# Optimization experiments

Measured on AMD Instinct MI355X. Metric: run time of the kernel, lower is better.

Reference implementation:

```python
import jax, jax.numpy as jnp
import numpy as np

NEG = 1e12  # matches the torch '-inf' surrogate value


def _sinusoidal_pos(seq_len, dim):
    # bert4keras-style: pe[..., 0::2] = sin, pe[..., 1::2] = cos
    pos = jnp.arange(seq_len, dtype=jnp.float32)
    i = jnp.arange(dim // 2, dtype=jnp.float32)
    freq = jnp.power(10000.0, -2.0 * i / dim)
    ang = pos[:, None] * freq[None, :]                      # [S, dim/2]
    pe = jnp.stack([jnp.sin(ang), jnp.cos(ang)], axis=-1)   # [S, dim/2, 2]
    return pe.reshape(seq_len, dim)                          # [S, dim]


def _rope(e, cos_pos, sin_pos):
    # additional_part = stack([-e[...,1::2], e[...,::2]], -1).reshape(e.shape)
    rot = jnp.stack([-e[..., 1::2], e[..., 0::2]], axis=-1).reshape(e.shape)
    return e * cos_pos + rot * sin_pos


def setup_inputs() -> dict:
    key = jax.random.key(0)
    k = jax.random.split(key, 5)
    B, S, H, inner, L = 8, 512, 768, 64, 16
    x = jax.random.normal(k[0], (B, S, H), dtype=jnp.float32)
    W1 = jax.random.normal(k[1], (H, 2 * inner), dtype=jnp.float32) * 0.02
    b1 = jnp.zeros((2 * inner,), dtype=jnp.float32)
    W2 = jax.random.normal(k[2], (H, 2 * L), dtype=jnp.float32) * 0.02
    b2 = jnp.zeros((2 * L,), dtype=jnp.float32)
    attention_mask = jnp.ones((B, S), dtype=jnp.int32)
    return {"x": x, "W1": W1, "b1": b1, "W2": W2, "b2": b2,
            "attention_mask": attention_mask}


def reference(x, W1, b1, W2, b2, attention_mask):
    B, S, H = x.shape
    inner = W1.shape[1] // 2

    t = x @ W1 + b1                                 # [B,S,2*inner]
    start_token = t[..., 0::2]                      # [B,S,inner]
    end_token = t[..., 1::2]                        # [B,S,inner]

    pe = _sinusoidal_pos(S, inner)[None]            # [1,S,inner]
    cos_pos = jnp.repeat(pe[..., 1::2], 2, axis=-1)
    sin_pos = jnp.repeat(pe[..., 0::2], 2, axis=-1)
    start_token = _rope(start_token, cos_pos, sin_pos)
    end_token = _rope(end_token, cos_pos, sin_pos)

    span_score = jnp.einsum('bmd,bnd->bmn', start_token, end_token) / (inner ** 0.5)

    typing = jnp.swapaxes(x @ W2 + b2, 1, 2) / 2.0  # [B,2L,S]

    # entity_score: [B, L, S(start), S(end)]
    entity_score = (span_score[:, None]
                    + typing[:, 0::2, None, :]
                    + typing[:, 1::2, :, None])

    m = attention_mask.astype(entity_score.dtype)
    m_row = m[:, None, :, None]                     # mask over start axis
    m_col = m[:, None, None, :]                     # mask over end axis
    entity_score = entity_score * m_row + (-NEG) * (1.0 - m_row)
    entity_score = entity_score * m_col + (-NEG) * (1.0 - m_col)

    tril = jnp.tril(jnp.ones((S, S), entity_score.dtype), k=-1)
    entity_score = entity_score - tril * NEG
    return entity_score
```

## Files before the change

kernel.cpp:

```cpp
#include <hip/hip_runtime.h>

#define NEGF 1.0e12f

constexpr int Hdim = 768;
constexpr int NC   = 160;
constexpr int ROWS = 4096;
constexpr int SEQ  = 512;
constexpr int KSPLIT = 4;

typedef __attribute__((ext_vector_type(8))) short  short8;
typedef __attribute__((ext_vector_type(4))) float  floatx4;

__device__ inline unsigned short f2bf(float f) {
    union { float f; unsigned u; } v; v.f = f;
    return (unsigned short)((v.u + 0x8000u) >> 16);
}

__global__ __launch_bounds__(256) void wprep_k(
    const float* __restrict__ W1, const float* __restrict__ W2,
    unsigned short* __restrict__ Wt)
{
    __shared__ __align__(16) unsigned short tile[160][72];
    const int tid = threadIdx.x;
    const int k0  = blockIdx.x * 64;

    for (int t = tid; t < 64 * 32; t += 256) {
        int k  = t >> 5;
        int c4 = (t & 31) * 4;
        float4 v = *(const float4*)(W1 + (size_t)(k0 + k) * 128 + c4);
        tile[c4 + 0][k] = f2bf(v.x); tile[c4 + 1][k] = f2bf(v.y);
        tile[c4 + 2][k] = f2bf(v.z); tile[c4 + 3][k] = f2bf(v.w);
    }
    for (int t = tid; t < 64 * 8; t += 256) {
        int k  = t >> 3;
        int c4 = (t & 7) * 4;
        float4 v = *(const float4*)(W2 + (size_t)(k0 + k) * 32 + c4);
        tile[128 + c4 + 0][k] = f2bf(v.x); tile[128 + c4 + 1][k] = f2bf(v.y);
        tile[128 + c4 + 2][k] = f2bf(v.z); tile[128 + c4 + 3][k] = f2bf(v.w);
    }
    __syncthreads();
    for (int t = tid; t < 160 * 8; t += 256) {
        int c  = t >> 3;
        int kq = (t & 7) * 8;
        short8 v = *(const short8*)(&tile[c][kq]);
        *(short8*)(Wt + (size_t)c * 768 + k0 + kq) = v;
    }
}

__global__ __launch_bounds__(256) void gemm_mfma_k(
    const float* __restrict__ x, const unsigned short* __restrict__ Wt,
    float* __restrict__ partial)
{
    __shared__ __align__(16) unsigned short xs[64 * 40];
    __shared__ __align__(16) unsigned short ws[NC * 40];

    const int tid  = threadIdx.x;
    const int wave = tid >> 6;
    const int lane = tid & 63;
    const int quad = lane >> 4;
    const int nl   = lane & 15;
    const int r0   = blockIdx.x * 64;
    const int k0   = blockIdx.y * 192;

    floatx4 acc[10];
#pragma unroll
    for (int t = 0; t < 10; t++) acc[t] = (floatx4)(0.0f);

    for (int kt = 0; kt < 192; kt += 32) {
        const int kb = k0 + kt;
        {
            const int row = tid >> 2;
            const int kq  = (tid & 3) * 8;
            const float* xp = x + (size_t)(r0 + row) * Hdim + kb + kq;
            float4 v0 = *(const float4*)xp;
            float4 v1 = *(const float4*)(xp + 4);
            short8 sv;
            sv[0] = (short)f2bf(v0.x); sv[1] = (short)f2bf(v0.y);
            sv[2] = (short)f2bf(v0.z); sv[3] = (short)f2bf(v0.w);
            sv[4] = (short)f2bf(v1.x); sv[5] = (short)f2bf(v1.y);
            sv[6] = (short)f2bf(v1.z); sv[7] = (short)f2bf(v1.w);
            *(short8*)(xs + row * 40 + kq) = sv;
        }
#pragma unroll
        for (int g = 0; g < 3; g++) {
            int task = g * 256 + tid;
            if (task < 640) {
                int c  = task >> 2;
                int kq = (task & 3) * 8;
                *(short8*)(ws + c * 40 + kq) =
                    *(const short8*)(Wt + (size_t)c * 768 + kb + kq);
            }
        }
        __syncthreads();

        short8 af = *(const short8*)(xs + (wave * 16 + nl) * 40 + quad * 8);
#pragma unroll
        for (int t = 0; t < 10; t++) {
            short8 bf = *(const short8*)(ws + (t * 16 + nl) * 40 + quad * 8);
            acc[t] = __builtin_amdgcn_mfma_f32_16x16x32_bf16(af, bf, acc[t], 0, 0, 0);
        }
        __syncthreads();
    }

    float* pout = partial + (size_t)blockIdx.y * ROWS * NC;
#pragma unroll
    for (int t = 0; t < 10; t++) {
#pragma unroll
        for (int r = 0; r < 4; r++) {
            pout[(size_t)(r0 + wave * 16 + quad * 4 + r) * NC + t * 16 + nl] = acc[t][r];
        }
    }
}

__global__ __launch_bounds__(256) void combine_rope_k(
    const float* __restrict__ partial, const float* __restrict__ b1,
    const float* __restrict__ b2, unsigned short* __restrict__ startbf,
    unsigned short* __restrict__ endbf, float* __restrict__ tyn,
    float* __restrict__ tym)
{
    const int tid = threadIdx.x;
    const int row = blockIdx.x * 4 + (tid >> 6);
    const int u   = tid & 63;
    const int b   = row >> 9;
    const int s   = row & 511;
    const float* p0 = partial + (size_t)row * NC;
    const size_t cstride = (size_t)ROWS * NC;

    if (u < 32) {
        const int i = u;
        float4 a0 = *(const float4*)(p0 + 4 * i);
        float4 a1 = *(const float4*)(p0 + cstride + 4 * i);
        float4 a2 = *(const float4*)(p0 + 2 * cstride + 4 * i);
        float4 a3 = *(const float4*)(p0 + 3 * cstride + 4 * i);
        float t0 = a0.x + a1.x + a2.x + a3.x + b1[4 * i + 0];
        float t1 = a0.y + a1.y + a2.y + a3.y + b1[4 * i + 1];
        float t2 = a0.z + a1.z + a2.z + a3.z + b1[4 * i + 2];
        float t3 = a0.w + a1.w + a2.w + a3.w + b1[4 * i + 3];
        float freq = __powf(10000.0f, -(float)i * (1.0f / 32.0f));
        float ang  = (float)s * freq;
        float sn, cs;
        __sincosf(ang, &sn, &cs);
        float so0 = (t0 * cs - t2 * sn) * 0.125f;
        float so1 = (t2 * cs + t0 * sn) * 0.125f;
        float eo0 = t1 * cs - t3 * sn;
        float eo1 = t3 * cs + t1 * sn;
        ushort2 sp; sp.x = f2bf(so0); sp.y = f2bf(so1);
        ushort2 ep; ep.x = f2bf(eo0); ep.y = f2bf(eo1);
        *(ushort2*)(startbf + (size_t)row * 64 + 2 * i) = sp;
        *(ushort2*)(endbf   + (size_t)row * 64 + 2 * i) = ep;
    } else {
        const int j = u - 32;
        float t = p0[128 + j] + p0[cstride + 128 + j] + p0[2 * cstride + 128 + j]
                + p0[3 * cstride + 128 + j] + b2[j];
        float v = t * 0.5f;
        const int l = j >> 1;
        if ((j & 1) == 0) tyn[((size_t)b * 16 + l) * SEQ + s] = v;
        else              tym[((size_t)b * 16 + l) * SEQ + s] = v;
    }
}

__global__ __launch_bounds__(256) void entity_k(
    const unsigned short* __restrict__ startbf, const unsigned short* __restrict__ endbf,
    const float* __restrict__ tyn, const float* __restrict__ tym,
    const int* __restrict__ amask, float* __restrict__ out)
{
    __shared__ __align__(16) unsigned short sA[64 * 72];
    __shared__ __align__(16) unsigned short sB[64 * 72];
    __shared__ float tyn_s[16 * 64];
    __shared__ float tym_s[16 * 64];
    __shared__ float mrow_s[64];
    __shared__ float mcol_s[64];

    const int tid = threadIdx.x;
    const int b   = blockIdx.z;
    const int m0  = blockIdx.y * 64;
    const int n0  = blockIdx.x * 64;

    for (int t = tid; t < 512; t += 256) {
        int row = t >> 3;
        int kq  = (t & 7) * 8;
        *(short8*)(sA + row * 72 + kq) =
            *(const short8*)(startbf + (size_t)(b * SEQ + m0 + row) * 64 + kq);
        *(short8*)(sB + row * 72 + kq) =
            *(const short8*)(endbf + (size_t)(b * SEQ + n0 + row) * 64 + kq);
    }
    for (int t = tid; t < 16 * 64; t += 256) {
        int l = t >> 6, i = t & 63;
        tym_s[t] = tym[((size_t)b * 16 + l) * SEQ + m0 + i];
        tyn_s[t] = tyn[((size_t)b * 16 + l) * SEQ + n0 + i];
    }
    if (tid < 64)       mrow_s[tid] = (float)amask[b * SEQ + m0 + tid];
    else if (tid < 128) mcol_s[tid - 64] = (float)amask[b * SEQ + n0 + (tid - 64)];
    __syncthreads();

    const int wave = tid >> 6;
    const int lane = tid & 63;
    const int quad = lane >> 4;
    const int nl   = lane & 15;

    short8 a0 = *(const short8*)(sA + (wave * 16 + nl) * 72 + quad * 8);
    short8 a1 = *(const short8*)(sA + (wave * 16 + nl) * 72 + 32 + quad * 8);

    floatx4 acc[4];
#pragma unroll
    for (int t = 0; t < 4; t++) acc[t] = (floatx4)(0.0f);
#pragma unroll
    for (int t = 0; t < 4; t++) {
        short8 bf0 = *(const short8*)(sB + (t * 16 + nl) * 72 + quad * 8);
        short8 bf1 = *(const short8*)(sB + (t * 16 + nl) * 72 + 32 + quad * 8);
        acc[t] = __builtin_amdgcn_mfma_f32_16x16x32_bf16(a0, bf0, acc[t], 0, 0, 0);
        acc[t] = __builtin_amdgcn_mfma_f32_16x16x32_bf16(a1, bf1, acc[t], 0, 0, 0);
    }

    float mr[4], radd[4];
#pragma unroll
    for (int r = 0; r < 4; r++) {
        mr[r]   = mrow_s[wave * 16 + quad * 4 + r];
        radd[r] = -NEGF * (1.0f - mr[r]);
    }
    float mc[4], cadd[4];
#pragma unroll
    for (int t = 0; t < 4; t++) {
        mc[t]   = mcol_s[t * 16 + nl];
        cadd[t] = -NEGF * (1.0f - mc[t]);
    }
    const bool lower = (m0 > n0);
    const bool diag  = (m0 == n0);
    const int  lm    = wave * 16 + quad * 4;

    for (int l = 0; l < 16; l++) {
        float tmv[4];
#pragma unroll
        for (int r = 0; r < 4; r++) tmv[r] = tym_s[l * 64 + lm + r];
        float* ob = out + ((size_t)(b * 16 + l) * SEQ + m0 + lm) * SEQ + n0;
#pragma unroll
        for (int t = 0; t < 4; t++) {
            float tnv = tyn_s[l * 64 + t * 16 + nl];
#pragma unroll
            for (int r = 0; r < 4; r++) {
                float v = acc[t][r] + tnv + tmv[r];
                v = v * mr[r] + radd[r];
                v = v * mc[t] + cadd[t];
                if (lower) v -= NEGF;
                else if (diag && (lm + r > t * 16 + nl)) v -= NEGF;
                ob[(size_t)r * SEQ + t * 16 + nl] = v;
            }
        }
    }
}

extern "C" void kernel_launch(void* const* d_in, const int* in_sizes, int n_in,
                              void* d_out, int out_size, void* d_ws, size_t ws_size,
                              hipStream_t stream) {
    const float* x     = (const float*)d_in[0];
    const float* W1    = (const float*)d_in[1];
    const float* b1    = (const float*)d_in[2];
    const float* W2    = (const float*)d_in[3];
    const float* b2    = (const float*)d_in[4];
    const int*   amask = (const int*)d_in[5];
    float* out = (float*)d_out;

    char* base = (char*)d_ws;
    unsigned short* Wt      = (unsigned short*)base;
    float*          partial = (float*)(base + 262144);
    unsigned short* startbf = (unsigned short*)(base + 262144 + 10485760);
    unsigned short* endbf   = (unsigned short*)(base + 262144 + 10485760 + 524288);
    float*          tyn     = (float*)(base + 262144 + 10485760 + 2 * 524288);
    float*          tym     = (float*)(base + 262144 + 10485760 + 2 * 524288 + 262144);

    hipLaunchKernelGGL(wprep_k, dim3(12), dim3(256), 0, stream, W1, W2, Wt);
    hipLaunchKernelGGL(gemm_mfma_k, dim3(64, KSPLIT), dim3(256), 0, stream,
                       x, Wt, partial);
    hipLaunchKernelGGL(combine_rope_k, dim3(ROWS / 4), dim3(256), 0, stream,
                       partial, b1, b2, startbf, endbf, tyn, tym);
    hipLaunchKernelGGL(entity_k, dim3(8, 8, 8), dim3(256), 0, stream,
                       startbf, endbf, tyn, tym, amask, out);
}
```

Before: 177.4 us.

## Fuse split-K projection GEMM with RoPE combine and drop LDS staging in entity kernel

The projection GEMM now splits K across the 8 waves of one block and reduces the partials in shared memory, then applies bias, RoPE and typing scaling in the same kernel. This removes the 10 MB partial buffer round-trip through global memory and one kernel launch. The entity kernel now loads its MFMA operands, typing values and mask directly from global memory into registers instead of staging them in LDS behind a barrier. The trade-off is only 256 GEMM blocks, each doing a small amount of work, and uncoalesced, repeated global reads in the entity kernel that rely on cache hits.

```diff
diff --git a/kernel.cpp b/kernel.cpp
--- a/kernel.cpp
+++ b/kernel.cpp
@@ -6,7 +6,6 @@
 constexpr int NC   = 160;
 constexpr int ROWS = 4096;
 constexpr int SEQ  = 512;
-constexpr int KSPLIT = 4;
 
 typedef __attribute__((ext_vector_type(8))) short  short8;
 typedef __attribute__((ext_vector_type(4))) float  floatx4;
@@ -47,115 +46,96 @@
     }
 }
 
-__global__ __launch_bounds__(256) void gemm_mfma_k(
+__global__ __launch_bounds__(512) void gemm_rope_k(
     const float* __restrict__ x, const unsigned short* __restrict__ Wt,
-    float* __restrict__ partial)
+    const float* __restrict__ b1, const float* __restrict__ b2,
+    unsigned short* __restrict__ startbf, unsigned short* __restrict__ endbf,
+    float* __restrict__ tyn, float* __restrict__ tym)
 {
-    __shared__ __align__(16) unsigned short xs[64 * 40];
-    __shared__ __align__(16) unsigned short ws[NC * 40];
+    __shared__ __align__(16) float ts[8 * 16 * 160];
 
     const int tid  = threadIdx.x;
     const int wave = tid >> 6;
     const int lane = tid & 63;
     const int quad = lane >> 4;
     const int nl   = lane & 15;
-    const int r0   = blockIdx.x * 64;
-    const int k0   = blockIdx.y * 192;
+    const int r0   = blockIdx.x * 16;
+    const int kbase = wave * 96;
 
     floatx4 acc[10];
 #pragma unroll
     for (int t = 0; t < 10; t++) acc[t] = (floatx4)(0.0f);
 
-    for (int kt = 0; kt < 192; kt += 32) {
-        const int kb = k0 + kt;
-        {
-            const int row = tid >> 2;
-            const int kq  = (tid & 3) * 8;
-            const float* xp = x + (size_t)(r0 + row) * Hdim + kb + kq;
-            float4 v0 = *(const float4*)xp;
-            float4 v1 = *(const float4*)(xp + 4);
-            short8 sv;
-            sv[0] = (short)f2bf(v0.x); sv[1] = (short)f2bf(v0.y);
-            sv[2] = (short)f2bf(v0.z); sv[3] = (short)f2bf(v0.w);
-            sv[4] = (short)f2bf(v1.x); sv[5] = (short)f2bf(v1.y);
-            sv[6] = (short)f2bf(v1.z); sv[7] = (short)f2bf(v1.w);
-            *(short8*)(xs + row * 40 + kq) = sv;
+#pragma unroll
+    for (int it = 0; it < 3; it++) {
+        const int kw = kbase + it * 32;
+        const float* xp = x + (size_t)(r0 + nl) * Hdim + kw + quad * 8;
+        float4 xa = *(const float4*)xp;
+        float4 xb = *(const float4*)(xp + 4);
+        short8 wr[10];
+#pragma unroll
+        for (int t = 0; t < 10; t++)
+            wr[t] = *(const short8*)(Wt + (size_t)(t * 16 + nl) * Hdim + kw + quad * 8);
+
+        short8 af;
+        af[0] = (short)f2bf(xa.x); af[1] = (short)f2bf(xa.y);
+        af[2] = (short)f2bf(xa.z); af[3] = (short)f2bf(xa.w);
+        af[4] = (short)f2bf(xb.x); af[5] = (short)f2bf(xb.y);
+        af[6] = (short)f2bf(xb.z); af[7] = (short)f2bf(xb.w);
+#pragma unroll
+        for (int t = 0; t < 10; t++)
+            acc[t] = __builtin_amdgcn_mfma_f32_16x16x32_bf16(af, wr[t], acc[t], 0, 0, 0);
+    }
+
+#pragma unroll
+    for (int t = 0; t < 10; t++) {
+#pragma unroll
+        for (int r = 0; r < 4; r++) {
+            ts[(wave * 16 + quad * 4 + r) * 160 + t * 16 + nl] = acc[t][r];
         }
-#pragma unroll
-        for (int g = 0; g < 3; g++) {
-            int task = g * 256 + tid;
-            if (task < 640) {
-                int c  = task >> 2;
-                int kq = (task & 3) * 8;
-                *(short8*)(ws + c * 40 + kq) =
-                    *(const short8*)(Wt + (size_t)c * 768 + kb + kq);
+    }
+    __syncthreads();
+
+#pragma unroll
+    for (int p = 0; p < 2; p++) {
+        const int unit = tid + p * 512;
+        const int lrow = unit >> 6;
+        const int u    = unit & 63;
+        const int grow = r0 + lrow;
+        const int b    = grow >> 9;
+        const int s    = grow & 511;
+        if (u < 32) {
+            const int i = u;
+            float t0 = 0.0f, t1 = 0.0f, t2 = 0.0f, t3 = 0.0f;
+#pragma unroll
+            for (int w = 0; w < 8; w++) {
+                float4 v = *(const float4*)(ts + (w * 16 + lrow) * 160 + 4 * i);
+                t0 += v.x; t1 += v.y; t2 += v.z; t3 += v.w;
             }
+            float4 bv = *(const float4*)(b1 + 4 * i);
+            t0 += bv.x; t1 += bv.y; t2 += bv.z; t3 += bv.w;
+            float freq = __powf(10000.0f, -(float)i * (1.0f / 32.0f));
+            float ang  = (float)s * freq;
+            float sn, cs;
+            __sincosf(ang, &sn, &cs);
+            float so0 = (t0 * cs - t2 * sn) * 0.125f;
+            float so1 = (t2 * cs + t0 * sn) * 0.125f;
+            float eo0 = t1 * cs - t3 * sn;
+            float eo1 = t3 * cs + t1 * sn;
+            ushort2 sp; sp.x = f2bf(so0); sp.y = f2bf(so1);
+            ushort2 ep; ep.x = f2bf(eo0); ep.y = f2bf(eo1);
+            *(ushort2*)(startbf + (size_t)grow * 64 + 2 * i) = sp;
+            *(ushort2*)(endbf   + (size_t)grow * 64 + 2 * i) = ep;
+        } else {
+            const int j = u - 32;
+            float t = 0.0f;
+#pragma unroll
+            for (int w = 0; w < 8; w++) t += ts[(w * 16 + lrow) * 160 + 128 + j];
+            float v = (t + b2[j]) * 0.5f;
+            const int l = j >> 1;
+            if ((j & 1) == 0) tyn[((size_t)b * 16 + l) * SEQ + s] = v;
+            else              tym[((size_t)b * 16 + l) * SEQ + s] = v;
         }
-        __syncthreads();
-
-        short8 af = *(const short8*)(xs + (wave * 16 + nl) * 40 + quad * 8);
-#pragma unroll
-        for (int t = 0; t < 10; t++) {
-            short8 bf = *(const short8*)(ws + (t * 16 + nl) * 40 + quad * 8);
-            acc[t] = __builtin_amdgcn_mfma_f32_16x16x32_bf16(af, bf, acc[t], 0, 0, 0);
-        }
-        __syncthreads();
-    }
-
-    float* pout = partial + (size_t)blockIdx.y * ROWS * NC;
-#pragma unroll
-    for (int t = 0; t < 10; t++) {
-#pragma unroll
-        for (int r = 0; r < 4; r++) {
-            pout[(size_t)(r0 + wave * 16 + quad * 4 + r) * NC + t * 16 + nl] = acc[t][r];
-        }
-    }
-}
-
-__global__ __launch_bounds__(256) void combine_rope_k(
-    const float* __restrict__ partial, const float* __restrict__ b1,
-    const float* __restrict__ b2, unsigned short* __restrict__ startbf,
-    unsigned short* __restrict__ endbf, float* __restrict__ tyn,
-    float* __restrict__ tym)
-{
-    const int tid = threadIdx.x;
-    const int row = blockIdx.x * 4 + (tid >> 6);
-    const int u   = tid & 63;
-    const int b   = row >> 9;
-    const int s   = row & 511;
-    const float* p0 = partial + (size_t)row * NC;
-    const size_t cstride = (size_t)ROWS * NC;
-
-    if (u < 32) {
-        const int i = u;
-        float4 a0 = *(const float4*)(p0 + 4 * i);
-        float4 a1 = *(const float4*)(p0 + cstride + 4 * i);
-        float4 a2 = *(const float4*)(p0 + 2 * cstride + 4 * i);
-        float4 a3 = *(const float4*)(p0 + 3 * cstride + 4 * i);
-        float t0 = a0.x + a1.x + a2.x + a3.x + b1[4 * i + 0];
-        float t1 = a0.y + a1.y + a2.y + a3.y + b1[4 * i + 1];
-        float t2 = a0.z + a1.z + a2.z + a3.z + b1[4 * i + 2];
-        float t3 = a0.w + a1.w + a2.w + a3.w + b1[4 * i + 3];
-        float freq = __powf(10000.0f, -(float)i * (1.0f / 32.0f));
-        float ang  = (float)s * freq;
-        float sn, cs;
-        __sincosf(ang, &sn, &cs);
-        float so0 = (t0 * cs - t2 * sn) * 0.125f;
-        float so1 = (t2 * cs + t0 * sn) * 0.125f;
-        float eo0 = t1 * cs - t3 * sn;
-        float eo1 = t3 * cs + t1 * sn;
-        ushort2 sp; sp.x = f2bf(so0); sp.y = f2bf(so1);
-        ushort2 ep; ep.x = f2bf(eo0); ep.y = f2bf(eo1);
-        *(ushort2*)(startbf + (size_t)row * 64 + 2 * i) = sp;
-        *(ushort2*)(endbf   + (size_t)row * 64 + 2 * i) = ep;
-    } else {
-        const int j = u - 32;
-        float t = p0[128 + j] + p0[cstride + 128 + j] + p0[2 * cstride + 128 + j]
-                + p0[3 * cstride + 128 + j] + b2[j];
-        float v = t * 0.5f;
-        const int l = j >> 1;
-        if ((j & 1) == 0) tyn[((size_t)b * 16 + l) * SEQ + s] = v;
-        else              tym[((size_t)b * 16 + l) * SEQ + s] = v;
     }
 }
 
@@ -164,82 +144,64 @@
     const float* __restrict__ tyn, const float* __restrict__ tym,
     const int* __restrict__ amask, float* __restrict__ out)
 {
-    __shared__ __align__(16) unsigned short sA[64 * 72];
-    __shared__ __align__(16) unsigned short sB[64 * 72];
-    __shared__ float tyn_s[16 * 64];
-    __shared__ float tym_s[16 * 64];
-    __shared__ float mrow_s[64];
-    __shared__ float mcol_s[64];
-
     const int tid = threadIdx.x;
     const int b   = blockIdx.z;
     const int m0  = blockIdx.y * 64;
     const int n0  = blockIdx.x * 64;
 
-    for (int t = tid; t < 512; t += 256) {
-        int row = t >> 3;
-        int kq  = (t & 7) * 8;
-        *(short8*)(sA + row * 72 + kq) =
-            *(const short8*)(startbf + (size_t)(b * SEQ + m0 + row) * 64 + kq);
-        *(short8*)(sB + row * 72 + kq) =
-            *(const short8*)(endbf + (size_t)(b * SEQ + n0 + row) * 64 + kq);
-    }
-    for (int t = tid; t < 16 * 64; t += 256) {
-        int l = t >> 6, i = t & 63;
-        tym_s[t] = tym[((size_t)b * 16 + l) * SEQ + m0 + i];
-        tyn_s[t] = tyn[((size_t)b * 16 + l) * SEQ + n0 + i];
-    }
-    if (tid < 64)       mrow_s[tid] = (float)amask[b * SEQ + m0 + tid];
-    else if (tid < 128) mcol_s[tid - 64] = (float)amask[b * SEQ + n0 + (tid - 64)];
-    __syncthreads();
-
     const int wave = tid >> 6;
     const int lane = tid & 63;
     const int quad = lane >> 4;
     const int nl   = lane & 15;
-
-    short8 a0 = *(const short8*)(sA + (wave * 16 + nl) * 72 + quad * 8);
-    short8 a1 = *(const short8*)(sA + (wave * 16 + nl) * 72 + 32 + quad * 8);
+    const int lm   = wave * 16 + quad * 4;
+
+    const unsigned short* arow = startbf + (size_t)(b * SEQ + m0 + wave * 16 + nl) * 64 + quad * 8;
+    short8 a0 = *(const short8*)arow;
+    short8 a1 = *(const short8*)(arow + 32);
 
     floatx4 acc[4];
 #pragma unroll
     for (int t = 0; t < 4; t++) acc[t] = (floatx4)(0.0f);
 #pragma unroll
     for (int t = 0; t < 4; t++) {
-        short8 bf0 = *(const short8*)(sB + (t * 16 + nl) * 72 + quad * 8);
-        short8 bf1 = *(const short8*)(sB + (t * 16 + nl) * 72 + 32 + quad * 8);
+        const unsigned short* brow = endbf + (size_t)(b * SEQ + n0 + t * 16 + nl) * 64 + quad * 8;
+        short8 bf0 = *(const short8*)brow;
+        short8 bf1 = *(const short8*)(brow + 32);
         acc[t] = __builtin_amdgcn_mfma_f32_16x16x32_bf16(a0, bf0, acc[t], 0, 0, 0);
         acc[t] = __builtin_amdgcn_mfma_f32_16x16x32_bf16(a1, bf1, acc[t], 0, 0, 0);
     }
 
     float mr[4], radd[4];
-#pragma unroll
-    for (int r = 0; r < 4; r++) {
-        mr[r]   = mrow_s[wave * 16 + quad * 4 + r];
-        radd[r] = -NEGF * (1.0f - mr[r]);
+    {
+        int4 mi = *(const int4*)(amask + b * SEQ + m0 + lm);
+        mr[0] = (float)mi.x; mr[1] = (float)mi.y; mr[2] = (float)mi.z; mr[3] = (float)mi.w;
+#pragma unroll
+        for (int r = 0; r < 4; r++) radd[r] = -NEGF * (1.0f - mr[r]);
     }
     float mc[4], cadd[4];
 #pragma unroll
     for (int t = 0; t < 4; t++) {
-        mc[t]   = mcol_s[t * 16 + nl];
+        mc[t]   = (float)amask[b * SEQ + n0 + t * 16 + nl];
         cadd[t] = -NEGF * (1.0f - mc[t]);
     }
     const bool lower = (m0 > n0);
     const bool diag  = (m0 == n0);
-    const int  lm    = wave * 16 + quad * 4;
 
     for (int l = 0; l < 16; l++) {
-        float tmv[4];
-#pragma unroll
-        for (int r = 0; r < 4; r++) tmv[r] = tym_s[l * 64 + lm + r];
+        float4 tmv = *(const float4*)(tym + ((size_t)b * 16 + l) * SEQ + m0 + lm);
+        float tnv[4];
+#pragma unroll
+        for (int t = 0; t < 4; t++)
+            tnv[t] = tyn[((size_t)b * 16 + l) * SEQ + n0 + t * 16 + nl];
         float* ob = out + ((size_t)(b * 16 + l) * SEQ + m0 + lm) * SEQ + n0;
 #pragma unroll
         for (int t = 0; t < 4; t++) {
-            float tnv = tyn_s[l * 64 + t * 16 + nl];
 #pragma unroll
             for (int r = 0; r < 4; r++) {
-                float v = acc[t][r] + tnv + tmv[r];
-                v = v * mr[r] + radd[r];
+                float tm = (r == 0) ? tmv.x : (r == 1) ? tmv.y : (r == 2) ? tmv.z : tmv.w;
+                float v = acc[t][r] + tnv[t] + tm;
+                v = v * ((r == 0) ? mr[0] : (r == 1) ? mr[1] : (r == 2) ? mr[2] : mr[3])
+                      + ((r == 0) ? radd[0] : (r == 1) ? radd[1] : (r == 2) ? radd[2] : radd[3]);
                 v = v * mc[t] + cadd[t];
                 if (lower) v -= NEGF;
                 else if (diag && (lm + r > t * 16 + nl)) v -= NEGF;
@@ -262,17 +224,14 @@
 
     char* base = (char*)d_ws;
     unsigned short* Wt      = (unsigned short*)base;
-    float*          partial = (float*)(base + 262144);
-    unsigned short* startbf = (unsigned short*)(base + 262144 + 10485760);
-    unsigned short* endbf   = (unsigned short*)(base + 262144 + 10485760 + 524288);
-    float*          tyn     = (float*)(base + 262144 + 10485760 + 2 * 524288);
-    float*          tym     = (float*)(base + 262144 + 10485760 + 2 * 524288 + 262144);
+    unsigned short* startbf = (unsigned short*)(base + 262144);
+    unsigned short* endbf   = (unsigned short*)(base + 262144 + 524288);
+    float*          tyn     = (float*)(base + 262144 + 2 * 524288);
+    float*          tym     = (float*)(base + 262144 + 2 * 524288 + 262144);
 
     hipLaunchKernelGGL(wprep_k, dim3(12), dim3(256), 0, stream, W1, W2, Wt);
-    hipLaunchKernelGGL(gemm_mfma_k, dim3(64, KSPLIT), dim3(256), 0, stream,
-                       x, Wt, partial);
-    hipLaunchKernelGGL(combine_rope_k, dim3(ROWS / 4), dim3(256), 0, stream,
-                       partial, b1, b2, startbf, endbf, tyn, tym);
+    hipLaunchKernelGGL(gemm_rope_k, dim3(256), dim3(512), 0, stream,
+                       x, Wt, b1, b2, startbf, endbf, tyn, tym);
     hipLaunchKernelGGL(entity_k, dim3(8, 8, 8), dim3(256), 0, stream,
                        startbf, endbf, tyn, tym, amask, out);
 }
```

New measurement: 170.0 us. 4.1% less time.
